# Performance work log

Measured on AMD Instinct MI355X. Metric: run time of the kernel, lower is better.

The kernel has to match this reference:

```python
import jax, jax.numpy as jnp
import numpy as np

C = 64          # in_channel
K = 3           # kernel_size
STRIDE = 1
PAD = 1


def make_weight():
    # torch.diag(ones(k*k)).repeat(C,1).reshape(C*k*k, 1, K, K)
    kk = K * K
    return jnp.tile(jnp.eye(kk, dtype=jnp.float32), (C, 1)).reshape(C * kk, 1, K, K)


def setup_inputs() -> dict:
    key = jax.random.key(0)
    x = jax.random.normal(key, (16, C, 112, 112), dtype=jnp.float32)
    return {"x": x, "weight": make_weight()}


def reference(x, weight):
    # Depthwise (grouped) conv with fixed diagonal-identity kernel == patch unfold.
    # Output: [N, C*K*K, H_out, W_out]
    return jax.lax.conv_general_dilated(
        x, weight,
        window_strides=(STRIDE, STRIDE),
        padding=[(PAD, PAD), (PAD, PAD)],
        dimension_numbers=("NCHW", "OIHW", "NCHW"),
        feature_group_count=C,
    )
```

## Files before the change

### kernel.cpp

```cpp
#include <hip/hip_runtime.h>


#define NN 16
#define CC 64
#define HH 112
#define WW 112
#define KK 9
#define W4 (WW / 4)

__global__ __launch_bounds__(256) void unfold_kernel(const float* __restrict__ x,
                                                     float* __restrict__ out,
                                                     unsigned total4) {
    unsigned idx = blockIdx.x * 256u + threadIdx.x;
    if (idx >= total4) return;

    unsigned w4 = idx % W4;
    unsigned t  = idx / W4;
    unsigned h  = t % HH;
    t /= HH;
    unsigned cj = t % (CC * KK);
    unsigned n  = t / (CC * KK);
    unsigned c  = cj / KK;
    unsigned j  = cj % KK;

    int dh = (int)(j / 3u) - 1;
    int dw = (int)(j % 3u) - 1;
    int sh = (int)h + dh;

    float4 v = make_float4(0.f, 0.f, 0.f, 0.f);
    if (sh >= 0 && sh < HH) {
        const float* __restrict__ src = x + ((((size_t)n * CC + c) * HH + (unsigned)sh) * WW);
        int base = (int)(w4 * 4u) + dw;
        float r[4];
#pragma unroll
        for (int e = 0; e < 4; ++e) {
            int sw = base + e;
            r[e] = (sw >= 0 && sw < WW) ? src[sw] : 0.f;
        }
        v = make_float4(r[0], r[1], r[2], r[3]);
    }
    reinterpret_cast<float4*>(out)[idx] = v;
}

extern "C" void kernel_launch(void* const* d_in, const int* in_sizes, int n_in,
                              void* d_out, int out_size, void* d_ws, size_t ws_size,
                              hipStream_t stream) {
    const float* x = (const float*)d_in[0];
    float* out = (float*)d_out;

    const unsigned total4 = (unsigned)(NN * CC * KK * HH * W4);
    const unsigned blocks = (total4 + 255u) / 256u;
    unfold_kernel<<<blocks, 256, 0, stream>>>(x, out, total4);
}
```

Before: 544.0 us.

## Compute all nine unfold taps per thread from shared row loads

Each thread now handles one (n,c,h,w4) position and produces all nine output planes. It loads three input rows as one vector each plus two edge scalars per row, builds the shifted vectors in registers, and replaces the earlier per-tap unaligned scalar loads and redundant reads. Output writes use nontemporal stores to avoid polluting cache. The grid shrinks ninefold and each thread does more work and issues writes to nine strided planes.

```diff
diff --git a/kernel.cpp b/kernel.cpp
--- a/kernel.cpp
+++ b/kernel.cpp
@@ -5,50 +5,62 @@
 #define CC 64
 #define HH 112
 #define WW 112
-#define KK 9
-#define W4 (WW / 4)
+#define W4C 28
+#define PLANE4 (HH * W4C)
 
-__global__ __launch_bounds__(256) void unfold_kernel(const float* __restrict__ x,
-                                                     float* __restrict__ out,
-                                                     unsigned total4) {
+typedef float v4f __attribute__((ext_vector_type(4)));
+
+__global__ __launch_bounds__(256) void unfold9_kernel(const float* __restrict__ x,
+                                                      v4f* __restrict__ out,
+                                                      unsigned total) {
     unsigned idx = blockIdx.x * 256u + threadIdx.x;
-    if (idx >= total4) return;
+    if (idx >= total) return;
 
-    unsigned w4 = idx % W4;
-    unsigned t  = idx / W4;
+    unsigned w4 = idx % W4C;
+    unsigned t  = idx / W4C;
     unsigned h  = t % HH;
     t /= HH;
-    unsigned cj = t % (CC * KK);
-    unsigned n  = t / (CC * KK);
-    unsigned c  = cj / KK;
-    unsigned j  = cj % KK;
+    unsigned c  = t % CC;
+    unsigned n  = t / CC;
 
-    int dh = (int)(j / 3u) - 1;
-    int dw = (int)(j % 3u) - 1;
-    int sh = (int)h + dh;
+    const float* __restrict__ xc = x + (((size_t)n * CC + c) * HH) * WW;
+    unsigned wbase = w4 * 4u;
 
-    float4 v = make_float4(0.f, 0.f, 0.f, 0.f);
-    if (sh >= 0 && sh < HH) {
-        const float* __restrict__ src = x + ((((size_t)n * CC + c) * HH + (unsigned)sh) * WW);
-        int base = (int)(w4 * 4u) + dw;
-        float r[4];
+    v4f   mid[3];
+    float lft[3], rgt[3];
 #pragma unroll
-        for (int e = 0; e < 4; ++e) {
-            int sw = base + e;
-            r[e] = (sw >= 0 && sw < WW) ? src[sw] : 0.f;
-        }
-        v = make_float4(r[0], r[1], r[2], r[3]);
+    for (int kr = 0; kr < 3; ++kr) {
+        int sh = (int)h + kr - 1;
+        bool ok = (sh >= 0) && (sh < HH);
+        const float* __restrict__ row = xc + (unsigned)(ok ? sh : 0) * WW;
+        v4f   m = *reinterpret_cast<const v4f*>(row + wbase);
+        float l = (w4 > 0u)        ? row[wbase - 1u] : 0.f;
+        float r = (w4 < W4C - 1u)  ? row[wbase + 4u] : 0.f;
+        if (!ok) { m = (v4f){0.f, 0.f, 0.f, 0.f}; l = 0.f; r = 0.f; }
+        mid[kr] = m; lft[kr] = l; rgt[kr] = r;
     }
-    reinterpret_cast<float4*>(out)[idx] = v;
+
+    size_t base = ((size_t)n * (CC * 9) + (size_t)c * 9) * PLANE4
+                + (size_t)h * W4C + w4;
+#pragma unroll
+    for (int kr = 0; kr < 3; ++kr) {
+        v4f m = mid[kr];
+        v4f a = (v4f){lft[kr], m.x, m.y, m.z};
+        v4f b = m;
+        v4f d = (v4f){m.y, m.z, m.w, rgt[kr]};
+        __builtin_nontemporal_store(a, &out[base + (size_t)(kr * 3 + 0) * PLANE4]);
+        __builtin_nontemporal_store(b, &out[base + (size_t)(kr * 3 + 1) * PLANE4]);
+        __builtin_nontemporal_store(d, &out[base + (size_t)(kr * 3 + 2) * PLANE4]);
+    }
 }
 
 extern "C" void kernel_launch(void* const* d_in, const int* in_sizes, int n_in,
                               void* d_out, int out_size, void* d_ws, size_t ws_size,
                               hipStream_t stream) {
     const float* x = (const float*)d_in[0];
-    float* out = (float*)d_out;
+    v4f* out = (v4f*)d_out;
 
-    const unsigned total4 = (unsigned)(NN * CC * KK * HH * W4);
-    const unsigned blocks = (total4 + 255u) / 256u;
-    unfold_kernel<<<blocks, 256, 0, stream>>>(x, out, total4);
+    const unsigned total = (unsigned)(NN * CC * HH * W4C);
+    const unsigned blocks = (total + 255u) / 256u;
+    unfold9_kernel<<<blocks, 256, 0, stream>>>(x, out, total);
 }
```

Measured after the change: 474.7 us. -12.7%, faster.
